# Performance work log

Hardware: AMD Instinct MI355X
Metric: run time of the kernel (lower is better)

## Reference

```python
import jax, jax.numpy as jnp
import numpy as np

B, N, D, K = 16, 1024, 512, 8
NUM_ITERS = 3
EPS = 1e-08
LN_EPS = 1e-05


def layer_norm(x, g, b):
    m = jnp.mean(x, axis=-1, keepdims=True)
    v = jnp.var(x, axis=-1, keepdims=True)
    return (x - m) * jax.lax.rsqrt(v + LN_EPS) * g + b


def setup_inputs() -> dict:
    key = jax.random.key(0)
    ks = jax.random.split(key, 8)
    s = 1.0 / np.sqrt(D)
    return {
        "embeddings": jax.random.normal(ks[0], (B, N, D), jnp.float32),
        "noise_init": jax.random.normal(ks[1], (B, K, D), jnp.float32),
        "noise_final": jax.random.normal(ks[2], (B, K, D), jnp.float32),
        "slots_mu": jax.random.normal(ks[3], (1, K, D), jnp.float32) * s,
        "slots_logsigma": jax.random.normal(ks[4], (1, K, D), jnp.float32) * s,
        "mixing_coeffs": jnp.ones((1, K), jnp.float32) / K,
        "Wk": jax.random.normal(ks[5], (D, D), jnp.float32) * s,
        "bk": jnp.zeros((D,), jnp.float32),
        "Wq": jax.random.normal(ks[6], (D, D), jnp.float32) * s,
        "bq": jnp.zeros((D,), jnp.float32),
        "Wv": jax.random.normal(ks[7], (D, D), jnp.float32) * s,
        "bv": jnp.zeros((D,), jnp.float32),
        "ln_g": jnp.ones((D,), jnp.float32),
        "ln_b": jnp.zeros((D,), jnp.float32),
    }


def reference(embeddings, noise_init, noise_final, slots_mu, slots_logsigma,
              mixing_coeffs, Wk, bk, Wq, bq, Wv, bv, ln_g, ln_b):
    b, n, d = embeddings.shape
    mixing = jnp.broadcast_to(mixing_coeffs, (b, K))           # [B,K]
    mu = jnp.broadcast_to(slots_mu, (b, K, d))                 # [B,K,D]
    sigma = jnp.exp(jnp.broadcast_to(slots_logsigma, (b, K, d)))
    slots = mu + sigma * noise_init                            # sampled slots

    x = layer_norm(embeddings, ln_g, ln_b)
    keys = x @ Wk + bk                                         # [B,N,D]
    values = x @ Wv + bv                                       # [B,N,D]
    # slots are never updated inside the loop, so queries are loop-invariant
    queries = slots @ Wq + bq                                  # [B,K,D]

    log2pi = jnp.float32(np.log(2.0 * np.pi))
    attn = None
    for _ in range(NUM_ITERS):
        diff = keys[:, :, None, :] - queries[:, None, :, :]    # [B,N,K,D]
        gll = -0.5 * jnp.sum(diff * diff / (sigma[:, None] ** 2 + EPS), axis=-1)  # [B,N,K]
        gll = (-0.5 * d * log2pi
               - 0.5 * jnp.sum(jnp.log(jnp.abs(sigma) + EPS), axis=-1)[:, None, :]
               + gll)
        attn = mixing[:, None, :] * gll                        # [B,N,K]
        attn = attn / jnp.sum(attn, axis=-1, keepdims=True)
        attn = attn / (jnp.sum(attn, axis=1, keepdims=True) + EPS)
        mu = jnp.einsum('bnk,bnd->bkd', attn, values)          # [B,K,D]
        diff2 = values[:, :, None, :] - mu[:, None, :, :]      # [B,N,K,D]
        sigma = jnp.einsum('bnk,bnkd->bkd', attn, diff2 * diff2)
        mixing = jnp.sum(attn, axis=1) / n

    sigma = jnp.maximum(jnp.abs(sigma), EPS)
    slots = mu + sigma * noise_final
    return slots, jnp.transpose(attn, (0, 2, 1))
```

## Files before the change

### kernel.cpp

```cpp
#include <hip/hip_runtime.h>
#include <math.h>

#define BB 16
#define NN 1024
#define DD 512
#define KK 8
#define EPS_ 1e-8f
#define LN_EPS_ 1e-5f
#define GLL_C0 (-470.4965290007924f)

typedef __attribute__((ext_vector_type(8))) short short8;
typedef __attribute__((ext_vector_type(4))) short short4v;
typedef __attribute__((ext_vector_type(4))) float f32x4;
typedef __attribute__((ext_vector_type(4))) int int4v;

static __device__ inline short f2bf(float f) {
    unsigned u = __builtin_bit_cast(unsigned, f);
    u = (u + 0x7fff + ((u >> 16) & 1)) >> 16;
    return (short)u;
}
static __device__ inline float bf2f(short s) {
    unsigned u = ((unsigned)(unsigned short)s) << 16;
    return __builtin_bit_cast(float, u);
}

struct Params {
    const float *emb, *noise_init, *noise_final, *slots_mu, *slots_logsg,
                *mixing_co, *Wk, *bk, *Wq, *bq, *Wv, *bv, *ln_g, *ln_b;
    float *out;
    float *queries, *attn, *s1p, *s2p, *off, *mix16, *colsum;
    short *Abf, *Kbf, *Vbf, *WtKV, *WqT, *slotbf, *F_bt;
};

__global__ __launch_bounds__(256) void k_pre(Params p)
{
    __shared__ __align__(16) short eb[4352];
    int u = blockIdx.x, tid = threadIdx.x;
    if (u < 4096) {
        int row  = u * 4 + (tid >> 6);
        int lane = tid & 63;
        const float* e = p.emb + (size_t)row * DD + lane * 8;
        float4 v0 = *(const float4*)e;
        float4 v1 = *(const float4*)(e + 4);
        float v[8] = {v0.x, v0.y, v0.z, v0.w, v1.x, v1.y, v1.z, v1.w};
        float s = 0.0f;
#pragma unroll
        for (int j = 0; j < 8; j++) s += v[j];
#pragma unroll
        for (int off = 32; off; off >>= 1) s += __shfl_xor(s, off);
        float m = s * (1.0f / DD);
        float vs = 0.0f;
#pragma unroll
        for (int j = 0; j < 8; j++) { float d = v[j] - m; vs = fmaf(d, d, vs); }
#pragma unroll
        for (int off = 32; off; off >>= 1) vs += __shfl_xor(vs, off);
        float rstd = rsqrtf(vs * (1.0f / DD) + LN_EPS_);

        float4 g0 = *(const float4*)&p.ln_g[lane * 8];
        float4 g1 = *(const float4*)&p.ln_g[lane * 8 + 4];
        float4 b0 = *(const float4*)&p.ln_b[lane * 8];
        float4 b1 = *(const float4*)&p.ln_b[lane * 8 + 4];
        float g[8] = {g0.x, g0.y, g0.z, g0.w, g1.x, g1.y, g1.z, g1.w};
        float bb[8] = {b0.x, b0.y, b0.z, b0.w, b1.x, b1.y, b1.z, b1.w};
        short8 o;
#pragma unroll
        for (int j = 0; j < 8; j++) o[j] = f2bf(fmaf((v[j] - m) * rstd, g[j], bb[j]));
        *(short8*)&p.Abf[(size_t)row * DD + lane * 8] = o;
    } else if (u < 4864) {
        int idx = u - 4096;
        int z = idx >> 8, rem = idx & 255;
        const float* W = (z == 0) ? p.Wk : (z == 1) ? p.Wv : p.Wq;
        short* T; int nbase;
        if (z < 2) { T = p.WtKV; nbase = z * 512; } else { T = p.WqT; nbase = 0; }
        int k0 = (rem & 15) * 32, n0 = (rem >> 4) * 32;
        int tx = tid & 31, ty = tid >> 5;
        float (*t)[33] = (float (*)[33])eb;
#pragma unroll
        for (int q = 0; q < 4; q++)
            t[ty + q * 8][tx] = W[(size_t)(k0 + ty + q * 8) * DD + n0 + tx];
        __syncthreads();
#pragma unroll
        for (int q = 0; q < 4; q++)
            T[(size_t)(nbase + n0 + ty + q * 8) * DD + k0 + tx] = f2bf(t[tx][ty + q * 8]);
    } else {
        int idx = u - 4864;
        int b = idx >> 3, k = idx & 7;
#pragma unroll
        for (int q = 0; q < 2; q++) {
            int d = tid + q * 256;
            float sg = expf(p.slots_logsg[k * DD + d]);
            float sl = fmaf(sg, p.noise_init[((size_t)(b * KK + k)) * DD + d],
                            p.slots_mu[k * DD + d]);
            p.slotbf[((size_t)(b * KK + k)) * DD + d] = f2bf(sl);
        }
    }
}

__global__ __launch_bounds__(256) void k_gemm(Params p)
{
    __shared__ __align__(16) short smem[32768];
    int u = blockIdx.x, tid = threadIdx.x;
    int w = tid >> 6, l = tid & 63;
    int x, by, qmode;
    if (u >= 1024) { qmode = 1; x = u - 1024; if (x >= 4) return; by = 128; }
    else           { qmode = 0; x = u >> 7;   by = u & 127; }
    const short* A  = qmode ? p.slotbf : p.Abf + (size_t)by * 128 * DD;
    const short* Bt = qmode ? p.WqT : p.WtKV;
    int row0 = qmode ? 0 : by * 128;
    int col0 = x * 128;

    int sr = l >> 3;
    int sg_off = ((l & 7) ^ sr) * 8;
    int mq = (w & 1) * 64, nq = (w >> 1) * 64;
    int fr = l & 15;
    int orow = (l >> 4) * 4, ocol = l & 15;

    auto STAGE = [&](int k0, int buf) {
        short* As_ = smem + buf * 8192;
        short* Bs_ = smem + 16384 + buf * 8192;
#pragma unroll
        for (int j = 0; j < 4; j++) {
            int rbj = w * 32 + j * 8;
            int r   = rbj + sr;
            __builtin_amdgcn_global_load_lds(
                (const __attribute__((address_space(1))) unsigned int*)
                    (A + (size_t)r * DD + k0 + sg_off),
                (__attribute__((address_space(3))) unsigned int*)
                    &As_[rbj * 64 + l * 8], 16, 0, 0);
            __builtin_amdgcn_global_load_lds(
                (const __attribute__((address_space(1))) unsigned int*)
                    (Bt + (size_t)(col0 + r) * DD + k0 + sg_off),
                (__attribute__((address_space(3))) unsigned int*)
                    &Bs_[rbj * 64 + l * 8], 16, 0, 0);
        }
    };

    f32x4 acc[4][4] = {};
    STAGE(0, 0);
    __syncthreads();
    for (int i = 0; i < 8; i++) {
        if (i < 7) STAGE((i + 1) * 64, (i + 1) & 1);
        const short* As_ = smem + (i & 1) * 8192;
        const short* Bs_ = smem + 16384 + (i & 1) * 8192;
#pragma unroll
        for (int kk = 0; kk < 2; kk++) {
            int g = kk * 4 + (l >> 4);
            short8 af[4], bfv[4];
#pragma unroll
            for (int mi = 0; mi < 4; mi++)
                af[mi] = *(const short8*)&As_[(mq + mi * 16 + fr) * 64 + (g ^ (fr & 7)) * 8];
#pragma unroll
            for (int ni = 0; ni < 4; ni++)
                bfv[ni] = *(const short8*)&Bs_[(nq + ni * 16 + fr) * 64 + (g ^ (fr & 7)) * 8];
#pragma unroll
            for (int mi = 0; mi < 4; mi++)
#pragma unroll
                for (int ni = 0; ni < 4; ni++)
                    acc[mi][ni] = __builtin_amdgcn_mfma_f32_16x16x32_bf16(
                        af[mi], bfv[ni], acc[mi][ni], 0, 0, 0);
        }
        __syncthreads();
    }

    float bvv[4];
#pragma unroll
    for (int ni = 0; ni < 4; ni++) {
        int col = col0 + nq + ni * 16 + ocol;
        bvv[ni] = qmode ? p.bq[col] : (x < 4 ? p.bk[col] : p.bv[col - 512]);
    }

    if (qmode) {
#pragma unroll
        for (int ni = 0; ni < 4; ni++) {
            int col = col0 + nq + ni * 16 + ocol;
#pragma unroll
            for (int mi = 0; mi < 4; mi++)
#pragma unroll
                for (int r = 0; r < 4; r++)
                    p.queries[(size_t)(mq + mi * 16 + orow + r) * DD + col] =
                        acc[mi][ni][r] + bvv[ni];
        }
    } else {
        short* eb = smem;
        short* dst = (x < 4) ? p.Kbf : p.Vbf;
        int ccol0 = (x & 3) * 128;
#pragma unroll
        for (int mi = 0; mi < 4; mi++)
#pragma unroll
            for (int r = 0; r < 4; r++) {
                int row = mq + mi * 16 + orow + r;
                int sw = ((row >> 2) & 3) << 1;
#pragma unroll
                for (int ni = 0; ni < 4; ni++) {
                    int colg = nq + ni * 16 + ocol;
                    eb[row * 128 + (((colg >> 3) ^ sw) * 8) + (colg & 7)] =
                        f2bf(acc[mi][ni][r] + bvv[ni]);
                }
            }
        __syncthreads();
#pragma unroll
        for (int i = 0; i < 8; i++) {
            int row = i * 16 + w * 4 + (l >> 4);
            int c = l & 15;
            int cc = c ^ (((row >> 2) & 3) << 1);
            short8 vv = *(const short8*)&eb[row * 128 + cc * 8];
            *(short8*)&dst[(size_t)(row0 + row) * 512 + ccol0 + c * 8] = vv;
        }
    }
}

__global__ __launch_bounds__(256) void k_fprep0(Params p)
{
    __shared__ float red[512];
    int u = blockIdx.x, tid = threadIdx.x;
    int b = u >> 4, k = u & 15;
    short* Fr = p.F_bt + (size_t)(b * 16 + k) * 1024;
    if (k >= KK) {
        short4v zv = {0, 0, 0, 0};
        *(short4v*)&Fr[tid * 4] = zv;
        if (tid == 0) { p.off[b * 16 + k] = 0.0f; p.mix16[b * 16 + k] = 0.0f; }
        return;
    }
    float* rc = red;
    float* rl = red + 256;
    float c = 0.0f, ld = 0.0f;
#pragma unroll
    for (int q = 0; q < 2; q++) {
        int d = tid * 2 + q;
        float sg = expf(p.slots_logsg[k * DD + d]);
        float iv = 1.0f / (sg * sg + EPS_);
        float qv = p.queries[((size_t)(b * KK + k)) * DD + d];
        Fr[d]       = f2bf(-0.5f * iv);
        Fr[512 + d] = f2bf(qv * iv);
        c  = fmaf(qv * qv, iv, c);
        ld += logf(fabsf(sg) + EPS_);
    }
    rc[tid] = c; rl[tid] = ld;
    __syncthreads();
    for (int s = 128; s > 0; s >>= 1) {
        if (tid < s) { rc[tid] += rc[tid + s]; rl[tid] += rl[tid + s]; }
        __syncthreads();
    }
    if (tid == 0) {
        p.off[b * 16 + k]    = GLL_C0 - 0.5f * rl[0] - 0.5f * rc[0];
        p.mix16[b * 16 + k]  = p.mixing_co[k];
        p.colsum[b * KK + k] = 0.0f;
    }
}

__global__ __launch_bounds__(512) void k_gllmu(Params p, int itlast)
{
    __shared__ f32x4 red[3][2][64];
    __shared__ float asml[32 * KK];
    int u = blockIdx.x, tid = threadIdx.x;
    int w = tid >> 6, l = tid & 63;
    int b = u >> 5, chunk = u & 31;
    int n0 = chunk * 32;
    int t = w & 1, ks = w >> 1;

    const short* Ka = p.Kbf + ((size_t)(b * NN + n0 + t * 16 + (l & 15))) * 512
                      + ks * 128 + (l >> 4) * 8;
    const short* Fi = p.F_bt + (size_t)(b * 16 + (l & 15)) * 1024
                      + ks * 128 + (l >> 4) * 8;
    f32x4 acc0 = {}, acc1 = {};
#pragma unroll
    for (int j = 0; j < 4; j++) {
        short8 kf = *(const short8*)&Ka[j * 32];
        short8 f0 = *(const short8*)&Fi[j * 32];
        short8 f1 = *(const short8*)&Fi[j * 32 + 512];
        short8 k2;
#pragma unroll
        for (int e = 0; e < 8; e++) {
            float kv = bf2f(kf[e]);
            k2[e] = f2bf(kv * kv);
        }
        acc0 = __builtin_amdgcn_mfma_f32_16x16x32_bf16(k2, f0, acc0, 0, 0, 0);
        acc1 = __builtin_amdgcn_mfma_f32_16x16x32_bf16(kf, f1, acc1, 0, 0, 0);
    }
    f32x4 acc = acc0 + acc1;

    if (ks) red[ks - 1][t][l] = acc;
    __syncthreads();
    if (ks == 0) {
#pragma unroll
        for (int i = 0; i < 3; i++) acc += red[i][t][l];
        int col = l & 15;
        int rloc = t * 16 + (l >> 4) * 4;
        float offv = p.off[b * 16 + col];
        float mixv = p.mix16[b * 16 + col];
        float a[4], den[4];
#pragma unroll
        for (int r = 0; r < 4; r++) {
            a[r] = mixv * (acc[r] + offv);
            den[r] = a[r];
        }
#pragma unroll
        for (int mask = 1; mask <= 8; mask <<= 1)
#pragma unroll
            for (int r = 0; r < 4; r++) den[r] += __shfl_xor(den[r], mask);
        float csl = 0.0f;
        if (col < KK) {
#pragma unroll
            for (int r = 0; r < 4; r++) {
                float vv = a[r] / den[r];
                asml[(rloc + r) * KK + col] = vv;
                if (itlast)
                    p.attn[((size_t)(b * NN + n0 + rloc + r)) * KK + col] = vv;
                csl += vv;
            }
        }
        csl += __shfl_xor(csl, 16);
        csl += __shfl_xor(csl, 32);
        if (l < KK) atomicAdd(&p.colsum[b * KK + l], csl);
    }
    __syncthreads();

    float s1[KK] = {}, s2[KK] = {};
    const short* vb = p.Vbf + ((size_t)(b * NN + n0)) * DD + tid;
#pragma unroll 4
    for (int nn = 0; nn < 32; nn++) {
        float v = bf2f(vb[(size_t)nn * DD]);
        float vq = v * v;
        float4 a0 = *(const float4*)&asml[nn * KK];
        float4 a1 = *(const float4*)&asml[nn * KK + 4];
        float aa[8] = {a0.x, a0.y, a0.z, a0.w, a1.x, a1.y, a1.z, a1.w};
#pragma unroll
        for (int k = 0; k < KK; k++) {
            s1[k] = fmaf(aa[k], v, s1[k]);
            s2[k] = fmaf(aa[k], vq, s2[k]);
        }
    }
    size_t base = ((size_t)(b * 32 + chunk) * KK) * DD + tid;
#pragma unroll
    for (int k = 0; k < KK; k++) {
        p.s1p[base + (size_t)k * DD] = s1[k];
        p.s2p[base + (size_t)k * DD] = s2[k];
    }
}

__global__ __launch_bounds__(256) void k_fprep(Params p)
{
    __shared__ float red[512];
    int u = blockIdx.x, tid = threadIdx.x;
    int b = u >> 3, k = u & 7;
    float cs   = p.colsum[b * KK + k];
    float inv  = 1.0f / (cs + EPS_);
    float ssum = cs * inv;
    short* Fr = p.F_bt + (size_t)(b * 16 + k) * 1024;
    float* rc = red;
    float* rl = red + 256;
    float c = 0.0f, ld = 0.0f;
#pragma unroll
    for (int q = 0; q < 2; q++) {
        int d = tid * 2 + q;
        float s1 = 0.0f, s2 = 0.0f;
#pragma unroll
        for (int ns = 0; ns < 32; ns++) {
            size_t o = ((size_t)(b * 32 + ns) * KK + k) * DD + d;
            s1 += p.s1p[o];
            s2 += p.s2p[o];
        }
        float m  = s1 * inv;
        float sg = s2 * inv - m * m * (2.0f - ssum);
        float iv = 1.0f / (sg * sg + EPS_);
        float qv = p.queries[((size_t)(b * KK + k)) * DD + d];
        Fr[d]       = f2bf(-0.5f * iv);
        Fr[512 + d] = f2bf(qv * iv);
        c  = fmaf(qv * qv, iv, c);
        ld += logf(fabsf(sg) + EPS_);
    }
    rc[tid] = c; rl[tid] = ld;
    __syncthreads();
    for (int s = 128; s > 0; s >>= 1) {
        if (tid < s) { rc[tid] += rc[tid + s]; rl[tid] += rl[tid + s]; }
        __syncthreads();
    }
    if (tid == 0) {
        p.off[b * 16 + k]    = GLL_C0 - 0.5f * rl[0] - 0.5f * rc[0];
        p.mix16[b * 16 + k]  = ssum * (1.0f / NN);
        p.colsum[b * KK + k] = 0.0f;
    }
}

__global__ __launch_bounds__(256) void k_final(Params p)
{
    int u = blockIdx.x, tid = threadIdx.x;
    if (u < 256) {
        int gid = u * 256 + tid;
        int d = gid & 511;
        int k = (gid >> 9) & 7;
        int b = gid >> 12;
        float s1 = 0.0f, s2 = 0.0f;
#pragma unroll
        for (int ns = 0; ns < 32; ns++) {
            size_t o = ((size_t)(b * 32 + ns) * KK + k) * DD + d;
            s1 += p.s1p[o];
            s2 += p.s2p[o];
        }
        float cs   = p.colsum[b * KK + k];
        float inv  = 1.0f / (cs + EPS_);
        float ssum = cs * inv;
        float m    = s1 * inv;
        float sg   = s2 * inv - m * m * (2.0f - ssum);
        p.out[gid] = fmaf(fmaxf(fabsf(sg), EPS_), p.noise_final[gid], m);
    } else {
        int gid = (u - 256) * 256 + tid;
        int b = gid >> 13;
        int k = (gid >> 10) & 7;
        int n = gid & 1023;
        float cs = p.colsum[b * KK + k];
        p.out[BB * KK * DD + gid] =
            p.attn[((size_t)(b * NN + n)) * KK + k] / (cs + EPS_);
    }
}

extern "C" void kernel_launch(void* const* d_in, const int* in_sizes, int n_in,
                              void* d_out, int out_size, void* d_ws, size_t ws_size,
                              hipStream_t stream)
{
    Params pp;
    pp.emb         = (const float*)d_in[0];
    pp.noise_init  = (const float*)d_in[1];
    pp.noise_final = (const float*)d_in[2];
    pp.slots_mu    = (const float*)d_in[3];
    pp.slots_logsg = (const float*)d_in[4];
    pp.mixing_co   = (const float*)d_in[5];
    pp.Wk          = (const float*)d_in[6];
    pp.bk          = (const float*)d_in[7];
    pp.Wq          = (const float*)d_in[8];
    pp.bq          = (const float*)d_in[9];
    pp.Wv          = (const float*)d_in[10];
    pp.bv          = (const float*)d_in[11];
    pp.ln_g        = (const float*)d_in[12];
    pp.ln_b        = (const float*)d_in[13];
    pp.out         = (float*)d_out;

    float* ws = (float*)d_ws;
    pp.queries = ws;
    pp.attn    = pp.queries + BB * KK * DD;
    pp.s1p     = pp.attn + BB * NN * KK;
    pp.s2p     = pp.s1p + (size_t)BB * 32 * KK * DD;
    pp.off     = pp.s2p + (size_t)BB * 32 * KK * DD;
    pp.mix16   = pp.off + BB * 16;
    pp.colsum  = pp.mix16 + BB * 16;
    pp.Abf     = (short*)(pp.colsum + BB * KK);
    pp.Kbf     = pp.Abf + (size_t)BB * NN * DD;
    pp.Vbf     = pp.Kbf + (size_t)BB * NN * DD;
    pp.WtKV    = pp.Vbf + (size_t)BB * NN * DD;
    pp.WqT     = pp.WtKV + (size_t)1024 * DD;
    pp.slotbf  = pp.WqT + (size_t)DD * DD;
    pp.F_bt    = pp.slotbf + (size_t)BB * KK * DD;

    k_pre<<<4992, 256, 0, stream>>>(pp);
    k_gemm<<<1032, 256, 0, stream>>>(pp);
    k_fprep0<<<256, 256, 0, stream>>>(pp);
    for (int it = 0; it < 3; it++) {
        k_gllmu<<<512, 512, 0, stream>>>(pp, it == 2);
        if (it < 2) k_fprep<<<128, 256, 0, stream>>>(pp);
    }
    k_final<<<768, 256, 0, stream>>>(pp);
}
```

Measured before the change: 196.0 us.

## Fuse F-prep into gllmu kernel and accumulate mu/sigma partials with atomics

Removes the separate k_fprep0 and k_fprep kernels. Each gllmu block now recomputes the per-slot F coefficients, offsets and mixing weights into shared memory, reading from triple-buffered per-iteration sums. The 32 per-chunk partial writes of s1/s2 become atomicAdds into a per-iteration buffer, and the buffers are zeroed inside the GEMM kernel and the preceding iteration. This drops four kernel launches and the strided 32-way partial reduction, at the cost of redundant F computation in every block (32 blocks per batch), heavy float atomic contention, and non-deterministic summation order.

```diff
diff --git a/kernel.cpp b/kernel.cpp
--- a/kernel.cpp
+++ b/kernel.cpp
@@ -28,8 +28,10 @@
     const float *emb, *noise_init, *noise_final, *slots_mu, *slots_logsg,
                 *mixing_co, *Wk, *bk, *Wq, *bq, *Wv, *bv, *ln_g, *ln_b;
     float *out;
-    float *queries, *attn, *s1p, *s2p, *off, *mix16, *colsum;
-    short *Abf, *Kbf, *Vbf, *WtKV, *WqT, *slotbf, *F_bt;
+    float *queries, *attn;
+    float *s1c, *s2c;
+    float *colsum;
+    short *Abf, *Kbf, *Vbf, *WtKV, *WqT, *slotbf;
 };
 
 __global__ __launch_bounds__(256) void k_pre(Params p)
@@ -102,8 +104,19 @@
     int u = blockIdx.x, tid = threadIdx.x;
     int w = tid >> 6, l = tid & 63;
     int x, by, qmode;
-    if (u >= 1024) { qmode = 1; x = u - 1024; if (x >= 4) return; by = 128; }
-    else           { qmode = 0; x = u >> 7;   by = u & 127; }
+    if (u >= 1024) {
+        qmode = 1; x = u - 1024;
+        if (x >= 4) {
+            int gidx = (x - 4) * 256 + tid;
+            for (int i = gidx; i < BB * KK * DD; i += 1024) {
+                p.s1c[i] = 0.0f;
+                p.s2c[i] = 0.0f;
+            }
+            if (gidx < BB * KK) p.colsum[gidx] = 0.0f;
+            return;
+        }
+        by = 128;
+    } else { qmode = 0; x = u >> 7; by = u & 127; }
     const short* A  = qmode ? p.slotbf : p.Abf + (size_t)by * 128 * DD;
     const short* Bt = qmode ? p.WqT : p.WtKV;
     int row0 = qmode ? 0 : by * 128;
@@ -209,65 +222,85 @@
     }
 }
 
-__global__ __launch_bounds__(256) void k_fprep0(Params p)
+__global__ __launch_bounds__(512) void k_gllmu(Params p, int it)
 {
-    __shared__ float red[512];
-    int u = blockIdx.x, tid = threadIdx.x;
-    int b = u >> 4, k = u & 15;
-    short* Fr = p.F_bt + (size_t)(b * 16 + k) * 1024;
-    if (k >= KK) {
-        short4v zv = {0, 0, 0, 0};
-        *(short4v*)&Fr[tid * 4] = zv;
-        if (tid == 0) { p.off[b * 16 + k] = 0.0f; p.mix16[b * 16 + k] = 0.0f; }
-        return;
-    }
-    float* rc = red;
-    float* rl = red + 256;
-    float c = 0.0f, ld = 0.0f;
-#pragma unroll
-    for (int q = 0; q < 2; q++) {
-        int d = tid * 2 + q;
-        float sg = expf(p.slots_logsg[k * DD + d]);
-        float iv = 1.0f / (sg * sg + EPS_);
-        float qv = p.queries[((size_t)(b * KK + k)) * DD + d];
-        Fr[d]       = f2bf(-0.5f * iv);
-        Fr[512 + d] = f2bf(qv * iv);
-        c  = fmaf(qv * qv, iv, c);
-        ld += logf(fabsf(sg) + EPS_);
-    }
-    rc[tid] = c; rl[tid] = ld;
-    __syncthreads();
-    for (int s = 128; s > 0; s >>= 1) {
-        if (tid < s) { rc[tid] += rc[tid + s]; rl[tid] += rl[tid + s]; }
-        __syncthreads();
-    }
-    if (tid == 0) {
-        p.off[b * 16 + k]    = GLL_C0 - 0.5f * rl[0] - 0.5f * rc[0];
-        p.mix16[b * 16 + k]  = p.mixing_co[k];
-        p.colsum[b * KK + k] = 0.0f;
-    }
-}
-
-__global__ __launch_bounds__(512) void k_gllmu(Params p, int itlast)
-{
+    __shared__ __align__(16) short F0L[16][520];
+    __shared__ __align__(16) short F1L[16][520];
     __shared__ f32x4 red[3][2][64];
     __shared__ float asml[32 * KK];
+    __shared__ float off_l[16], mix_l[16];
+
     int u = blockIdx.x, tid = threadIdx.x;
     int w = tid >> 6, l = tid & 63;
     int b = u >> 5, chunk = u & 31;
     int n0 = chunk * 32;
     int t = w & 1, ks = w >> 1;
 
+    if (it < 2) {
+        int gidx = u * 512 + tid;
+        if (gidx < BB * KK * DD) {
+            p.s1c[(it + 1) * (BB * KK * DD) + gidx] = 0.0f;
+            p.s2c[(it + 1) * (BB * KK * DD) + gidx] = 0.0f;
+        }
+        if (u == 0 && tid < BB * KK) p.colsum[(it + 1) * (BB * KK) + tid] = 0.0f;
+    }
+
+    {
+        int k = w;
+        const float* qrow = p.queries + ((size_t)(b * KK + k)) * DD;
+        float inv = 0.0f, ssum = 0.0f;
+        if (it > 0) {
+            float cs = p.colsum[(it - 1) * (BB * KK) + b * KK + k];
+            inv  = 1.0f / (cs + EPS_);
+            ssum = cs * inv;
+        }
+        float c = 0.0f, ld = 0.0f;
+        short8 f0v, f1v;
+#pragma unroll
+        for (int j = 0; j < 8; j++) {
+            int d = l * 8 + j;
+            float sg;
+            if (it == 0) {
+                sg = expf(p.slots_logsg[k * DD + d]);
+            } else {
+                float s1 = p.s1c[(it - 1) * (BB * KK * DD) + (b * KK + k) * DD + d];
+                float s2 = p.s2c[(it - 1) * (BB * KK * DD) + (b * KK + k) * DD + d];
+                float m  = s1 * inv;
+                sg = s2 * inv - m * m * (2.0f - ssum);
+            }
+            float iv = 1.0f / (sg * sg + EPS_);
+            float qv = qrow[d];
+            f0v[j] = f2bf(-0.5f * iv);
+            f1v[j] = f2bf(qv * iv);
+            c  = fmaf(qv * qv, iv, c);
+            ld += logf(fabsf(sg) + EPS_);
+        }
+        *(short8*)&F0L[k][l * 8] = f0v;
+        *(short8*)&F1L[k][l * 8] = f1v;
+        short8 zz = {};
+        *(short8*)&F0L[k + 8][l * 8] = zz;
+        *(short8*)&F1L[k + 8][l * 8] = zz;
+#pragma unroll
+        for (int m_ = 32; m_; m_ >>= 1) { c += __shfl_xor(c, m_); ld += __shfl_xor(ld, m_); }
+        if (l == 0) {
+            off_l[k] = GLL_C0 - 0.5f * ld - 0.5f * c;
+            mix_l[k] = (it == 0) ? p.mixing_co[k] : ssum * (1.0f / NN);
+            off_l[k + 8] = 0.0f;
+            mix_l[k + 8] = 0.0f;
+        }
+    }
+    __syncthreads();
+
     const short* Ka = p.Kbf + ((size_t)(b * NN + n0 + t * 16 + (l & 15))) * 512
                       + ks * 128 + (l >> 4) * 8;
-    const short* Fi = p.F_bt + (size_t)(b * 16 + (l & 15)) * 1024
-                      + ks * 128 + (l >> 4) * 8;
+    const short* F0r = &F0L[l & 15][ks * 128 + (l >> 4) * 8];
+    const short* F1r = &F1L[l & 15][ks * 128 + (l >> 4) * 8];
     f32x4 acc0 = {}, acc1 = {};
 #pragma unroll
     for (int j = 0; j < 4; j++) {
         short8 kf = *(const short8*)&Ka[j * 32];
-        short8 f0 = *(const short8*)&Fi[j * 32];
-        short8 f1 = *(const short8*)&Fi[j * 32 + 512];
+        short8 f0 = *(const short8*)&F0r[j * 32];
+        short8 f1 = *(const short8*)&F1r[j * 32];
         short8 k2;
 #pragma unroll
         for (int e = 0; e < 8; e++) {
@@ -286,8 +319,8 @@
         for (int i = 0; i < 3; i++) acc += red[i][t][l];
         int col = l & 15;
         int rloc = t * 16 + (l >> 4) * 4;
-        float offv = p.off[b * 16 + col];
-        float mixv = p.mix16[b * 16 + col];
+        float offv = off_l[col];
+        float mixv = mix_l[col];
         float a[4], den[4];
 #pragma unroll
         for (int r = 0; r < 4; r++) {
@@ -304,14 +337,14 @@
             for (int r = 0; r < 4; r++) {
                 float vv = a[r] / den[r];
                 asml[(rloc + r) * KK + col] = vv;
-                if (itlast)
+                if (it == 2)
                     p.attn[((size_t)(b * NN + n0 + rloc + r)) * KK + col] = vv;
                 csl += vv;
             }
         }
         csl += __shfl_xor(csl, 16);
         csl += __shfl_xor(csl, 32);
-        if (l < KK) atomicAdd(&p.colsum[b * KK + l], csl);
+        if (l < KK) atomicAdd(&p.colsum[it * (BB * KK) + b * KK + l], csl);
     }
     __syncthreads();
 
@@ -330,55 +363,12 @@
             s2[k] = fmaf(aa[k], vq, s2[k]);
         }
     }
-    size_t base = ((size_t)(b * 32 + chunk) * KK) * DD + tid;
+    float* s1d = p.s1c + it * (BB * KK * DD) + (size_t)b * KK * DD + tid;
+    float* s2d = p.s2c + it * (BB * KK * DD) + (size_t)b * KK * DD + tid;
 #pragma unroll
     for (int k = 0; k < KK; k++) {
-        p.s1p[base + (size_t)k * DD] = s1[k];
-        p.s2p[base + (size_t)k * DD] = s2[k];
-    }
-}
-
-__global__ __launch_bounds__(256) void k_fprep(Params p)
-{
-    __shared__ float red[512];
-    int u = blockIdx.x, tid = threadIdx.x;
-    int b = u >> 3, k = u & 7;
-    float cs   = p.colsum[b * KK + k];
-    float inv  = 1.0f / (cs + EPS_);
-    float ssum = cs * inv;
-    short* Fr = p.F_bt + (size_t)(b * 16 + k) * 1024;
-    float* rc = red;
-    float* rl = red + 256;
-    float c = 0.0f, ld = 0.0f;
-#pragma unroll
-    for (int q = 0; q < 2; q++) {
-        int d = tid * 2 + q;
-        float s1 = 0.0f, s2 = 0.0f;
-#pragma unroll
-        for (int ns = 0; ns < 32; ns++) {
-            size_t o = ((size_t)(b * 32 + ns) * KK + k) * DD + d;
-            s1 += p.s1p[o];
-            s2 += p.s2p[o];
-        }
-        float m  = s1 * inv;
-        float sg = s2 * inv - m * m * (2.0f - ssum);
-        float iv = 1.0f / (sg * sg + EPS_);
-        float qv = p.queries[((size_t)(b * KK + k)) * DD + d];
-        Fr[d]       = f2bf(-0.5f * iv);
-        Fr[512 + d] = f2bf(qv * iv);
-        c  = fmaf(qv * qv, iv, c);
-        ld += logf(fabsf(sg) + EPS_);
-    }
-    rc[tid] = c; rl[tid] = ld;
-    __syncthreads();
-    for (int s = 128; s > 0; s >>= 1) {
-        if (tid < s) { rc[tid] += rc[tid + s]; rl[tid] += rl[tid + s]; }
-        __syncthreads();
-    }
-    if (tid == 0) {
-        p.off[b * 16 + k]    = GLL_C0 - 0.5f * rl[0] - 0.5f * rc[0];
-        p.mix16[b * 16 + k]  = ssum * (1.0f / NN);
-        p.colsum[b * KK + k] = 0.0f;
+        atomicAdd(&s1d[(size_t)k * DD], s1[k]);
+        atomicAdd(&s2d[(size_t)k * DD], s2[k]);
     }
 }
 
@@ -387,17 +377,11 @@
     int u = blockIdx.x, tid = threadIdx.x;
     if (u < 256) {
         int gid = u * 256 + tid;
-        int d = gid & 511;
         int k = (gid >> 9) & 7;
         int b = gid >> 12;
-        float s1 = 0.0f, s2 = 0.0f;
-#pragma unroll
-        for (int ns = 0; ns < 32; ns++) {
-            size_t o = ((size_t)(b * 32 + ns) * KK + k) * DD + d;
-            s1 += p.s1p[o];
-            s2 += p.s2p[o];
-        }
-        float cs   = p.colsum[b * KK + k];
+        float s1 = p.s1c[2 * (BB * KK * DD) + gid];
+        float s2 = p.s2c[2 * (BB * KK * DD) + gid];
+        float cs   = p.colsum[2 * (BB * KK) + b * KK + k];
         float inv  = 1.0f / (cs + EPS_);
         float ssum = cs * inv;
         float m    = s1 * inv;
@@ -408,7 +392,7 @@
         int b = gid >> 13;
         int k = (gid >> 10) & 7;
         int n = gid & 1023;
-        float cs = p.colsum[b * KK + k];
+        float cs = p.colsum[2 * (BB * KK) + b * KK + k];
         p.out[BB * KK * DD + gid] =
             p.attn[((size_t)(b * NN + n)) * KK + k] / (cs + EPS_);
     }
@@ -438,25 +422,19 @@
     float* ws = (float*)d_ws;
     pp.queries = ws;
     pp.attn    = pp.queries + BB * KK * DD;
-    pp.s1p     = pp.attn + BB * NN * KK;
-    pp.s2p     = pp.s1p + (size_t)BB * 32 * KK * DD;
-    pp.off     = pp.s2p + (size_t)BB * 32 * KK * DD;
-    pp.mix16   = pp.off + BB * 16;
-    pp.colsum  = pp.mix16 + BB * 16;
-    pp.Abf     = (short*)(pp.colsum + BB * KK);
+    pp.s1c     = pp.attn + BB * NN * KK;
+    pp.s2c     = pp.s1c + 3 * BB * KK * DD;
+    pp.colsum  = pp.s2c + 3 * BB * KK * DD;
+    pp.Abf     = (short*)(pp.colsum + 3 * BB * KK);
     pp.Kbf     = pp.Abf + (size_t)BB * NN * DD;
     pp.Vbf     = pp.Kbf + (size_t)BB * NN * DD;
     pp.WtKV    = pp.Vbf + (size_t)BB * NN * DD;
     pp.WqT     = pp.WtKV + (size_t)1024 * DD;
     pp.slotbf  = pp.WqT + (size_t)DD * DD;
-    pp.F_bt    = pp.slotbf + (size_t)BB * KK * DD;
 
     k_pre<<<4992, 256, 0, stream>>>(pp);
     k_gemm<<<1032, 256, 0, stream>>>(pp);
-    k_fprep0<<<256, 256, 0, stream>>>(pp);
-    for (int it = 0; it < 3; it++) {
-        k_gllmu<<<512, 512, 0, stream>>>(pp, it == 2);
-        if (it < 2) k_fprep<<<128, 256, 0, stream>>>(pp);
-    }
+    for (int it = 0; it < 3; it++)
+        k_gllmu<<<512, 512, 0, stream>>>(pp, it);
     k_final<<<768, 256, 0, stream>>>(pp);
 }
```

After: 223.0 us. +13.8%, slower.

## Fold initial F/offset prep into pre and query GEMM; halve gllmu chunk count

Applied to the files above, without the earlier changes.

Removes the k_fprep0 launch. The log-sigma sum, padding zeroing and 1/sigma² table move into k_pre's slot blocks, and the query GEMM epilogue writes the F_bt rows and atomically adds the q²/sigma² term to the offsets. Separately, each k_gllmu block now processes 64 points instead of 32, which halves the grid and the partial-sum buffers that k_fprep and k_final reduce. The costs are fewer blocks for parallelism, two barrier rounds per block, scattered 2-byte stores and shared atomics in the small query-GEMM epilogue, and an ordering dependence of off on k_pre.

```diff
diff --git a/kernel.cpp b/kernel.cpp
--- a/kernel.cpp
+++ b/kernel.cpp
@@ -28,7 +28,10 @@
     const float *emb, *noise_init, *noise_final, *slots_mu, *slots_logsg,
                 *mixing_co, *Wk, *bk, *Wq, *bq, *Wv, *bv, *ln_g, *ln_b;
     float *out;
-    float *queries, *attn, *s1p, *s2p, *off, *mix16, *colsum;
+    float *queries, *attn;
+    float *s1p, *s2p;
+    float *off, *mix16, *colsum;
+    float *ivtab;
     short *Abf, *Kbf, *Vbf, *WtKV, *WqT, *slotbf, *F_bt;
 };
 
@@ -85,6 +88,8 @@
     } else {
         int idx = u - 4864;
         int b = idx >> 3, k = idx & 7;
+        float* redf = (float*)eb;
+        float ld = 0.0f;
 #pragma unroll
         for (int q = 0; q < 2; q++) {
             int d = tid + q * 256;
@@ -92,6 +97,25 @@
             float sl = fmaf(sg, p.noise_init[((size_t)(b * KK + k)) * DD + d],
                             p.slots_mu[k * DD + d]);
             p.slotbf[((size_t)(b * KK + k)) * DD + d] = f2bf(sl);
+            if (b == 0) p.ivtab[k * DD + d] = 1.0f / (sg * sg + EPS_);
+            ld += logf(fabsf(sg) + EPS_);
+        }
+        {
+            short4v zv = {0, 0, 0, 0};
+            *(short4v*)&p.F_bt[(size_t)(b * 16 + 8 + k) * 1024 + tid * 4] = zv;
+        }
+        redf[tid] = ld;
+        __syncthreads();
+        for (int s = 128; s > 0; s >>= 1) {
+            if (tid < s) redf[tid] += redf[tid + s];
+            __syncthreads();
+        }
+        if (tid == 0) {
+            p.off[b * 16 + k]       = GLL_C0 - 0.5f * redf[0];
+            p.mix16[b * 16 + k]     = p.mixing_co[k];
+            p.off[b * 16 + 8 + k]   = 0.0f;
+            p.mix16[b * 16 + 8 + k] = 0.0f;
+            p.colsum[b * KK + k]    = 0.0f;
         }
     }
 }
@@ -170,16 +194,29 @@
     }
 
     if (qmode) {
+        float* cpart = (float*)smem;
+        if (tid < 128) cpart[tid] = 0.0f;
+        __syncthreads();
 #pragma unroll
         for (int ni = 0; ni < 4; ni++) {
             int col = col0 + nq + ni * 16 + ocol;
 #pragma unroll
             for (int mi = 0; mi < 4; mi++)
 #pragma unroll
-                for (int r = 0; r < 4; r++)
-                    p.queries[(size_t)(mq + mi * 16 + orow + r) * DD + col] =
-                        acc[mi][ni][r] + bvv[ni];
-        }
+                for (int r = 0; r < 4; r++) {
+                    int row = mq + mi * 16 + orow + r;
+                    float qv = acc[mi][ni][r] + bvv[ni];
+                    p.queries[(size_t)row * DD + col] = qv;
+                    float iv = p.ivtab[(row & 7) * DD + col];
+                    int frow = (row >> 3) * 16 + (row & 7);
+                    p.F_bt[(size_t)frow * 1024 + col]       = f2bf(-0.5f * iv);
+                    p.F_bt[(size_t)frow * 1024 + 512 + col] = f2bf(qv * iv);
+                    atomicAdd(&cpart[row], qv * qv * iv);
+                }
+        }
+        __syncthreads();
+        if (tid < 128)
+            atomicAdd(&p.off[(tid >> 3) * 16 + (tid & 7)], -0.5f * cpart[tid]);
     } else {
         short* eb = smem;
         short* dst = (x < 4) ? p.Kbf : p.Vbf;
@@ -209,116 +246,80 @@
     }
 }
 
-__global__ __launch_bounds__(256) void k_fprep0(Params p)
-{
-    __shared__ float red[512];
-    int u = blockIdx.x, tid = threadIdx.x;
-    int b = u >> 4, k = u & 15;
-    short* Fr = p.F_bt + (size_t)(b * 16 + k) * 1024;
-    if (k >= KK) {
-        short4v zv = {0, 0, 0, 0};
-        *(short4v*)&Fr[tid * 4] = zv;
-        if (tid == 0) { p.off[b * 16 + k] = 0.0f; p.mix16[b * 16 + k] = 0.0f; }
-        return;
-    }
-    float* rc = red;
-    float* rl = red + 256;
-    float c = 0.0f, ld = 0.0f;
-#pragma unroll
-    for (int q = 0; q < 2; q++) {
-        int d = tid * 2 + q;
-        float sg = expf(p.slots_logsg[k * DD + d]);
-        float iv = 1.0f / (sg * sg + EPS_);
-        float qv = p.queries[((size_t)(b * KK + k)) * DD + d];
-        Fr[d]       = f2bf(-0.5f * iv);
-        Fr[512 + d] = f2bf(qv * iv);
-        c  = fmaf(qv * qv, iv, c);
-        ld += logf(fabsf(sg) + EPS_);
-    }
-    rc[tid] = c; rl[tid] = ld;
-    __syncthreads();
-    for (int s = 128; s > 0; s >>= 1) {
-        if (tid < s) { rc[tid] += rc[tid + s]; rl[tid] += rl[tid + s]; }
-        __syncthreads();
-    }
-    if (tid == 0) {
-        p.off[b * 16 + k]    = GLL_C0 - 0.5f * rl[0] - 0.5f * rc[0];
-        p.mix16[b * 16 + k]  = p.mixing_co[k];
-        p.colsum[b * KK + k] = 0.0f;
-    }
-}
-
 __global__ __launch_bounds__(512) void k_gllmu(Params p, int itlast)
 {
     __shared__ f32x4 red[3][2][64];
-    __shared__ float asml[32 * KK];
+    __shared__ float asml[64 * KK];
     int u = blockIdx.x, tid = threadIdx.x;
     int w = tid >> 6, l = tid & 63;
-    int b = u >> 5, chunk = u & 31;
-    int n0 = chunk * 32;
+    int b = u >> 4, chunk = u & 15;
+    int n0 = chunk * 64;
     int t = w & 1, ks = w >> 1;
 
-    const short* Ka = p.Kbf + ((size_t)(b * NN + n0 + t * 16 + (l & 15))) * 512
-                      + ks * 128 + (l >> 4) * 8;
-    const short* Fi = p.F_bt + (size_t)(b * 16 + (l & 15)) * 1024
-                      + ks * 128 + (l >> 4) * 8;
-    f32x4 acc0 = {}, acc1 = {};
-#pragma unroll
-    for (int j = 0; j < 4; j++) {
-        short8 kf = *(const short8*)&Ka[j * 32];
-        short8 f0 = *(const short8*)&Fi[j * 32];
-        short8 f1 = *(const short8*)&Fi[j * 32 + 512];
-        short8 k2;
-#pragma unroll
-        for (int e = 0; e < 8; e++) {
-            float kv = bf2f(kf[e]);
-            k2[e] = f2bf(kv * kv);
-        }
-        acc0 = __builtin_amdgcn_mfma_f32_16x16x32_bf16(k2, f0, acc0, 0, 0, 0);
-        acc1 = __builtin_amdgcn_mfma_f32_16x16x32_bf16(kf, f1, acc1, 0, 0, 0);
-    }
-    f32x4 acc = acc0 + acc1;
-
-    if (ks) red[ks - 1][t][l] = acc;
-    __syncthreads();
+    float csl = 0.0f;
+#pragma unroll
+    for (int st = 0; st < 2; st++) {
+        const short* Ka = p.Kbf
+            + ((size_t)(b * NN + n0 + st * 32 + t * 16 + (l & 15))) * 512
+            + ks * 128 + (l >> 4) * 8;
+        const short* Fi = p.F_bt + (size_t)(b * 16 + (l & 15)) * 1024
+            + ks * 128 + (l >> 4) * 8;
+        f32x4 acc0 = {}, acc1 = {};
+#pragma unroll
+        for (int j = 0; j < 4; j++) {
+            short8 kf = *(const short8*)&Ka[j * 32];
+            short8 f0 = *(const short8*)&Fi[j * 32];
+            short8 f1 = *(const short8*)&Fi[j * 32 + 512];
+            short8 k2;
+#pragma unroll
+            for (int e = 0; e < 8; e++) {
+                float kv = bf2f(kf[e]);
+                k2[e] = f2bf(kv * kv);
+            }
+            acc0 = __builtin_amdgcn_mfma_f32_16x16x32_bf16(k2, f0, acc0, 0, 0, 0);
+            acc1 = __builtin_amdgcn_mfma_f32_16x16x32_bf16(kf, f1, acc1, 0, 0, 0);
+        }
+        f32x4 acc = acc0 + acc1;
+
+        if (ks) red[ks - 1][t][l] = acc;
+        __syncthreads();
+        if (ks == 0) {
+#pragma unroll
+            for (int i = 0; i < 3; i++) acc += red[i][t][l];
+            int col = l & 15;
+            int rloc = st * 32 + t * 16 + (l >> 4) * 4;
+            float offv = p.off[b * 16 + col];
+            float mixv = p.mix16[b * 16 + col];
+            float a[4], den[4];
+#pragma unroll
+            for (int r = 0; r < 4; r++) { a[r] = mixv * (acc[r] + offv); den[r] = a[r]; }
+#pragma unroll
+            for (int mask = 1; mask <= 8; mask <<= 1)
+#pragma unroll
+                for (int r = 0; r < 4; r++) den[r] += __shfl_xor(den[r], mask);
+            if (col < KK) {
+#pragma unroll
+                for (int r = 0; r < 4; r++) {
+                    float vv = a[r] / den[r];
+                    asml[(rloc + r) * KK + col] = vv;
+                    if (itlast)
+                        p.attn[((size_t)(b * NN + n0 + rloc + r)) * KK + col] = vv;
+                    csl += vv;
+                }
+            }
+        }
+        __syncthreads();
+    }
     if (ks == 0) {
-#pragma unroll
-        for (int i = 0; i < 3; i++) acc += red[i][t][l];
-        int col = l & 15;
-        int rloc = t * 16 + (l >> 4) * 4;
-        float offv = p.off[b * 16 + col];
-        float mixv = p.mix16[b * 16 + col];
-        float a[4], den[4];
-#pragma unroll
-        for (int r = 0; r < 4; r++) {
-            a[r] = mixv * (acc[r] + offv);
-            den[r] = a[r];
-        }
-#pragma unroll
-        for (int mask = 1; mask <= 8; mask <<= 1)
-#pragma unroll
-            for (int r = 0; r < 4; r++) den[r] += __shfl_xor(den[r], mask);
-        float csl = 0.0f;
-        if (col < KK) {
-#pragma unroll
-            for (int r = 0; r < 4; r++) {
-                float vv = a[r] / den[r];
-                asml[(rloc + r) * KK + col] = vv;
-                if (itlast)
-                    p.attn[((size_t)(b * NN + n0 + rloc + r)) * KK + col] = vv;
-                csl += vv;
-            }
-        }
         csl += __shfl_xor(csl, 16);
         csl += __shfl_xor(csl, 32);
         if (l < KK) atomicAdd(&p.colsum[b * KK + l], csl);
     }
-    __syncthreads();
 
     float s1[KK] = {}, s2[KK] = {};
     const short* vb = p.Vbf + ((size_t)(b * NN + n0)) * DD + tid;
 #pragma unroll 4
-    for (int nn = 0; nn < 32; nn++) {
+    for (int nn = 0; nn < 64; nn++) {
         float v = bf2f(vb[(size_t)nn * DD]);
         float vq = v * v;
         float4 a0 = *(const float4*)&asml[nn * KK];
@@ -330,7 +331,7 @@
             s2[k] = fmaf(aa[k], vq, s2[k]);
         }
     }
-    size_t base = ((size_t)(b * 32 + chunk) * KK) * DD + tid;
+    size_t base = ((size_t)(b * 16 + chunk) * KK) * DD + tid;
 #pragma unroll
     for (int k = 0; k < KK; k++) {
         p.s1p[base + (size_t)k * DD] = s1[k];
@@ -355,8 +356,8 @@
         int d = tid * 2 + q;
         float s1 = 0.0f, s2 = 0.0f;
 #pragma unroll
-        for (int ns = 0; ns < 32; ns++) {
-            size_t o = ((size_t)(b * 32 + ns) * KK + k) * DD + d;
+        for (int ns = 0; ns < 16; ns++) {
+            size_t o = ((size_t)(b * 16 + ns) * KK + k) * DD + d;
             s1 += p.s1p[o];
             s2 += p.s2p[o];
         }
@@ -392,8 +393,8 @@
         int b = gid >> 12;
         float s1 = 0.0f, s2 = 0.0f;
 #pragma unroll
-        for (int ns = 0; ns < 32; ns++) {
-            size_t o = ((size_t)(b * 32 + ns) * KK + k) * DD + d;
+        for (int ns = 0; ns < 16; ns++) {
+            size_t o = ((size_t)(b * 16 + ns) * KK + k) * DD + d;
             s1 += p.s1p[o];
             s2 += p.s2p[o];
         }
@@ -439,11 +440,12 @@
     pp.queries = ws;
     pp.attn    = pp.queries + BB * KK * DD;
     pp.s1p     = pp.attn + BB * NN * KK;
-    pp.s2p     = pp.s1p + (size_t)BB * 32 * KK * DD;
-    pp.off     = pp.s2p + (size_t)BB * 32 * KK * DD;
+    pp.s2p     = pp.s1p + (size_t)BB * 16 * KK * DD;
+    pp.off     = pp.s2p + (size_t)BB * 16 * KK * DD;
     pp.mix16   = pp.off + BB * 16;
     pp.colsum  = pp.mix16 + BB * 16;
-    pp.Abf     = (short*)(pp.colsum + BB * KK);
+    pp.ivtab   = pp.colsum + BB * KK;
+    pp.Abf     = (short*)(pp.ivtab + KK * DD);
     pp.Kbf     = pp.Abf + (size_t)BB * NN * DD;
     pp.Vbf     = pp.Kbf + (size_t)BB * NN * DD;
     pp.WtKV    = pp.Vbf + (size_t)BB * NN * DD;
@@ -453,9 +455,8 @@
 
     k_pre<<<4992, 256, 0, stream>>>(pp);
     k_gemm<<<1032, 256, 0, stream>>>(pp);
-    k_fprep0<<<256, 256, 0, stream>>>(pp);
     for (int it = 0; it < 3; it++) {
-        k_gllmu<<<512, 512, 0, stream>>>(pp, it == 2);
+        k_gllmu<<<256, 512, 0, stream>>>(pp, it == 2);
         if (it < 2) k_fprep<<<128, 256, 0, stream>>>(pp);
     }
     k_final<<<768, 256, 0, stream>>>(pp);
```

Result: slower. 222.5 us (+13.5%).

## Fuse per-iteration fprep into gllmu via last-block atomic counter

Applied to the files above, without the earlier changes.

Removes the separate k_fprep launch between iterations. Each gllmu block bumps a per-batch atomic counter after its partial-sum writes, and the last block to finish for a batch performs the reduction and F/off/mix preparation. This saves two kernel launches and their gaps. In exchange, the reduction now runs on only 16 blocks (one per batch, 8 slots serial) instead of 128, which adds tail latency and needs threadfence/atomic ordering.

```diff
diff --git a/kernel.cpp b/kernel.cpp
--- a/kernel.cpp
+++ b/kernel.cpp
@@ -29,6 +29,7 @@
                 *mixing_co, *Wk, *bk, *Wq, *bq, *Wv, *bv, *ln_g, *ln_b;
     float *out;
     float *queries, *attn, *s1p, *s2p, *off, *mix16, *colsum;
+    int   *donecnt;
     short *Abf, *Kbf, *Vbf, *WtKV, *WqT, *slotbf, *F_bt;
 };
 
@@ -102,8 +103,15 @@
     int u = blockIdx.x, tid = threadIdx.x;
     int w = tid >> 6, l = tid & 63;
     int x, by, qmode;
-    if (u >= 1024) { qmode = 1; x = u - 1024; if (x >= 4) return; by = 128; }
-    else           { qmode = 0; x = u >> 7;   by = u & 127; }
+    if (u >= 1024) {
+        qmode = 1; x = u - 1024;
+        if (x >= 4) {
+            if (x == 4 && tid < 2 * BB) p.donecnt[tid] = 0;
+            return;
+        }
+        by = 128;
+    }
+    else { qmode = 0; x = u >> 7; by = u & 127; }
     const short* A  = qmode ? p.slotbf : p.Abf + (size_t)by * 128 * DD;
     const short* Bt = qmode ? p.WqT : p.WtKV;
     int row0 = qmode ? 0 : by * 128;
@@ -248,15 +256,18 @@
     }
 }
 
-__global__ __launch_bounds__(512) void k_gllmu(Params p, int itlast)
+__global__ __launch_bounds__(512) void k_gllmu(Params p, int it)
 {
     __shared__ f32x4 red[3][2][64];
     __shared__ float asml[32 * KK];
+    __shared__ int lastf;
+    __shared__ float redc[KK][8], redl[KK][8];
     int u = blockIdx.x, tid = threadIdx.x;
     int w = tid >> 6, l = tid & 63;
     int b = u >> 5, chunk = u & 31;
     int n0 = chunk * 32;
     int t = w & 1, ks = w >> 1;
+    int itlast = (it == 2);
 
     const short* Ka = p.Kbf + ((size_t)(b * NN + n0 + t * 16 + (l & 15))) * 512
                       + ks * 128 + (l >> 4) * 8;
@@ -336,49 +347,59 @@
         p.s1p[base + (size_t)k * DD] = s1[k];
         p.s2p[base + (size_t)k * DD] = s2[k];
     }
-}
-
-__global__ __launch_bounds__(256) void k_fprep(Params p)
-{
-    __shared__ float red[512];
-    int u = blockIdx.x, tid = threadIdx.x;
-    int b = u >> 3, k = u & 7;
-    float cs   = p.colsum[b * KK + k];
-    float inv  = 1.0f / (cs + EPS_);
-    float ssum = cs * inv;
-    short* Fr = p.F_bt + (size_t)(b * 16 + k) * 1024;
-    float* rc = red;
-    float* rl = red + 256;
-    float c = 0.0f, ld = 0.0f;
-#pragma unroll
-    for (int q = 0; q < 2; q++) {
-        int d = tid * 2 + q;
-        float s1 = 0.0f, s2 = 0.0f;
-#pragma unroll
-        for (int ns = 0; ns < 32; ns++) {
-            size_t o = ((size_t)(b * 32 + ns) * KK + k) * DD + d;
-            s1 += p.s1p[o];
-            s2 += p.s2p[o];
-        }
-        float m  = s1 * inv;
-        float sg = s2 * inv - m * m * (2.0f - ssum);
-        float iv = 1.0f / (sg * sg + EPS_);
-        float qv = p.queries[((size_t)(b * KK + k)) * DD + d];
-        Fr[d]       = f2bf(-0.5f * iv);
-        Fr[512 + d] = f2bf(qv * iv);
-        c  = fmaf(qv * qv, iv, c);
-        ld += logf(fabsf(sg) + EPS_);
-    }
-    rc[tid] = c; rl[tid] = ld;
-    __syncthreads();
-    for (int s = 128; s > 0; s >>= 1) {
-        if (tid < s) { rc[tid] += rc[tid + s]; rl[tid] += rl[tid + s]; }
-        __syncthreads();
-    }
-    if (tid == 0) {
-        p.off[b * 16 + k]    = GLL_C0 - 0.5f * rl[0] - 0.5f * rc[0];
-        p.mix16[b * 16 + k]  = ssum * (1.0f / NN);
-        p.colsum[b * KK + k] = 0.0f;
+
+    if (it < 2) {
+        __threadfence();
+        __syncthreads();
+        if (tid == 0) {
+            int old = __hip_atomic_fetch_add(&p.donecnt[it * BB + b], 1,
+                                             __ATOMIC_ACQ_REL,
+                                             __HIP_MEMORY_SCOPE_AGENT);
+            lastf = (old == 31);
+        }
+        __syncthreads();
+        if (!lastf) return;
+        int d = tid;
+        for (int k = 0; k < KK; k++) {
+            float cs   = p.colsum[b * KK + k];
+            float inv  = 1.0f / (cs + EPS_);
+            float ssum = cs * inv;
+            float s1v = 0.0f, s2v = 0.0f;
+#pragma unroll
+            for (int ns = 0; ns < 32; ns++) {
+                size_t o = ((size_t)(b * 32 + ns) * KK + k) * DD + d;
+                s1v += p.s1p[o];
+                s2v += p.s2p[o];
+            }
+            float m  = s1v * inv;
+            float sg = s2v * inv - m * m * (2.0f - ssum);
+            float iv = 1.0f / (sg * sg + EPS_);
+            float qv = p.queries[((size_t)(b * KK + k)) * DD + d];
+            short* Fr = p.F_bt + (size_t)(b * 16 + k) * 1024;
+            Fr[d]       = f2bf(-0.5f * iv);
+            Fr[512 + d] = f2bf(qv * iv);
+            float c  = qv * qv * iv;
+            float ld = logf(fabsf(sg) + EPS_);
+#pragma unroll
+            for (int m_ = 32; m_; m_ >>= 1) {
+                c  += __shfl_xor(c, m_);
+                ld += __shfl_xor(ld, m_);
+            }
+            if (l == 0) { redc[k][w] = c; redl[k][w] = ld; }
+        }
+        __syncthreads();
+        if (tid < KK) {
+            int k = tid;
+            float cs   = p.colsum[b * KK + k];
+            float inv  = 1.0f / (cs + EPS_);
+            float ssum = cs * inv;
+            float rc = 0.0f, rl = 0.0f;
+#pragma unroll
+            for (int i = 0; i < 8; i++) { rc += redc[k][i]; rl += redl[k][i]; }
+            p.off[b * 16 + k]    = GLL_C0 - 0.5f * rl - 0.5f * rc;
+            p.mix16[b * 16 + k]  = ssum * (1.0f / NN);
+            p.colsum[b * KK + k] = 0.0f;
+        }
     }
 }
 
@@ -443,7 +464,8 @@
     pp.off     = pp.s2p + (size_t)BB * 32 * KK * DD;
     pp.mix16   = pp.off + BB * 16;
     pp.colsum  = pp.mix16 + BB * 16;
-    pp.Abf     = (short*)(pp.colsum + BB * KK);
+    pp.donecnt = (int*)(pp.colsum + BB * KK);
+    pp.Abf     = (short*)(pp.donecnt + 2 * BB);
     pp.Kbf     = pp.Abf + (size_t)BB * NN * DD;
     pp.Vbf     = pp.Kbf + (size_t)BB * NN * DD;
     pp.WtKV    = pp.Vbf + (size_t)BB * NN * DD;
@@ -454,9 +476,7 @@
     k_pre<<<4992, 256, 0, stream>>>(pp);
     k_gemm<<<1032, 256, 0, stream>>>(pp);
     k_fprep0<<<256, 256, 0, stream>>>(pp);
-    for (int it = 0; it < 3; it++) {
-        k_gllmu<<<512, 512, 0, stream>>>(pp, it == 2);
-        if (it < 2) k_fprep<<<128, 256, 0, stream>>>(pp);
-    }
+    for (int it = 0; it < 3; it++)
+        k_gllmu<<<512, 512, 0, stream>>>(pp, it);
     k_final<<<768, 256, 0, stream>>>(pp);
 }
```

After: 670.8 us. 242% more time.
